# Kernel tuning notes

Hardware: AMD Instinct MI355X
Metric: run time of the kernel (lower is better)

Reference implementation:

```python
import jax, jax.numpy as jnp
import numpy as np

K = 8               # top-k frequencies
PRED_LEN = 96       # prediction_length
LOW_FREQ = 1        # low_frequency cutoff (drops DC)


def setup_inputs() -> dict:
    key = jax.random.key(0)
    x = jax.random.normal(key, (32, 2048, 64), dtype=jnp.float32)
    return {"x": x}


def reference(x):
    b, t, d = x.shape
    x_freq = jnp.fft.rfft(x, axis=1)                 # (b, t//2+1, d) complex
    freqs = jnp.fft.rfftfreq(t).astype(x.dtype)
    if t % 2 == 0:
        x_freq = x_freq[:, LOW_FREQ:-1]              # drop DC and Nyquist
        f = freqs[LOW_FREQ:-1]
    else:
        x_freq = x_freq[:, LOW_FREQ:]
        f = freqs[LOW_FREQ:]

    # top-k over frequency dim (axis=1), independently per (b, d)
    mag = jnp.abs(x_freq)                            # (b, F, d)
    _, idx = jax.lax.top_k(jnp.moveaxis(mag, 1, 2), K)  # (b, d, K), sorted desc
    idx = jnp.moveaxis(idx, 1, 2)                    # (b, K, d)
    x_k = jnp.take_along_axis(x_freq, idx, axis=1)   # (b, K, d) complex
    f_k = f[idx]                                     # (b, K, d)

    # extrapolate: add conjugate (negative) frequencies, then cos-sum
    x2 = jnp.concatenate([x_k, jnp.conj(x_k)], axis=1)  # (b, 2K, d)
    f2 = jnp.concatenate([f_k, -f_k], axis=1)           # (b, 2K, d)
    t_val = jnp.arange(t + PRED_LEN, dtype=x.dtype)     # (T,)
    amp = jnp.abs(x2) / t                               # (b, 2K, d)
    phase = jnp.angle(x2)                               # (b, 2K, d)
    # (b, 2K, T, d) broadcast intermediate, reduced over freq axis
    x_time = amp[:, :, None, :] * jnp.cos(
        2.0 * np.float32(np.pi) * f2[:, :, None, :] * t_val[None, None, :, None]
        + phase[:, :, None, :]
    )
    return x_time.sum(axis=1)                        # (b, t+PRED_LEN, d)
```

## Files before the change

### kernel.cpp

```cpp
#include <hip/hip_runtime.h>
#include <math.h>

#define BB 32
#define TT 2048
#define DD 64
#define PRED 96
#define TP (TT + PRED)
#define KTOP 8
#define NCAND 16
#define NSIG (BB * DD)
#define MARGIN 8e-4f
#define PI_D 3.14159265358979323846

__device__ __forceinline__ int physIdx(int idx) { return idx ^ ((idx >> 5) & 31); }

__device__ __forceinline__ int posOf(int k) {
    return ((k & 7) << 8) | (((k >> 3) & 7) << 5) | (((k >> 6) & 7) << 2) | (k >> 9);
}

__device__ __forceinline__ float2 cadd(float2 a, float2 b) { return make_float2(a.x + b.x, a.y + b.y); }
__device__ __forceinline__ float2 csub(float2 a, float2 b) { return make_float2(a.x - b.x, a.y - b.y); }
__device__ __forceinline__ float2 cmulni(float2 a) { return make_float2(a.y, -a.x); }
__device__ __forceinline__ float2 cmulpi(float2 a) { return make_float2(-a.y, a.x); }
__device__ __forceinline__ float2 cw8(float2 a) {
    const float s = 0.70710678118654752f;
    return make_float2(s * (a.x + a.y), s * (a.y - a.x));
}
__device__ __forceinline__ float2 cw83(float2 a) {
    const float s = 0.70710678118654752f;
    return make_float2(s * (a.y - a.x), -s * (a.x + a.y));
}
__device__ __forceinline__ float2 ctw(float2 a, int m) {
    const float rev = (float)m * (1.0f / 2048.0f);
    const float c = __builtin_amdgcn_cosf(rev);
    const float s = __builtin_amdgcn_sinf(rev);
    return make_float2(a.x * c + a.y * s, a.y * c - a.x * s);
}

__device__ __forceinline__ void radix8(float2* r) {
    float2 E0, E1, E2, E3, O0, O1, O2, O3;
    {
        float2 s0 = cadd(r[0], r[4]), s1 = csub(r[0], r[4]);
        float2 s2 = cadd(r[2], r[6]), s3 = csub(r[2], r[6]);
        E0 = cadd(s0, s2); E2 = csub(s0, s2);
        E1 = cadd(s1, cmulni(s3)); E3 = cadd(s1, cmulpi(s3));
    }
    {
        float2 s0 = cadd(r[1], r[5]), s1 = csub(r[1], r[5]);
        float2 s2 = cadd(r[3], r[7]), s3 = csub(r[3], r[7]);
        O0 = cadd(s0, s2); O2 = csub(s0, s2);
        O1 = cadd(s1, cmulni(s3)); O3 = cadd(s1, cmulpi(s3));
    }
    const float2 w1 = cw8(O1), w2 = cmulni(O2), w3 = cw83(O3);
    r[0] = cadd(E0, O0); r[4] = csub(E0, O0);
    r[1] = cadd(E1, w1); r[5] = csub(E1, w1);
    r[2] = cadd(E2, w2); r[6] = csub(E2, w2);
    r[3] = cadd(E3, w3); r[7] = csub(E3, w3);
}

__global__ __launch_bounds__(256) void fft_topk_kernel(const float* __restrict__ x,
                                                       int* __restrict__ idxw,
                                                       float* __restrict__ rew,
                                                       float* __restrict__ imw) {
    __shared__ float2 Z[TT];
    __shared__ int    candS[2][NCAND];
    __shared__ int    flagS[2];
    __shared__ double resR[2][NCAND], resI[2][NCAND], resM[2][NCAND];
    __shared__ double2 wA[32];
    __shared__ double2 wB[64];

    const int i    = blockIdx.x;
    const int xcd  = i & 7;
    const int slot = i >> 3;
    const int b    = xcd * 4 + (slot >> 5);
    const int dp   = slot & 31;
    const int t    = threadIdx.x;

    const float2* xv = (const float2*)x;
    const size_t base = (size_t)b * TT * (DD / 2) + dp;
    float2 r[8];
    #pragma unroll
    for (int q = 0; q < 8; ++q) r[q] = xv[base + (size_t)(t + 256 * q) * (DD / 2)];

    radix8(r);
    #pragma unroll
    for (int p = 1; p < 8; ++p) r[p] = ctw(r[p], (p * t) & (TT - 1));
    #pragma unroll
    for (int p = 0; p < 8; ++p) Z[physIdx(t + (p << 8))] = r[p];
    __syncthreads();

    const int S2 = (t >> 5) << 8, j2 = t & 31;
    #pragma unroll
    for (int p = 0; p < 8; ++p) r[p] = Z[physIdx(S2 + j2 + (p << 5))];
    radix8(r);
    #pragma unroll
    for (int p = 1; p < 8; ++p) r[p] = ctw(r[p], (8 * p * j2) & (TT - 1));
    #pragma unroll
    for (int p = 0; p < 8; ++p) Z[physIdx(S2 + j2 + (p << 5))] = r[p];
    __syncthreads();

    const int S3 = (t >> 2) << 5, j3 = t & 3;
    #pragma unroll
    for (int p = 0; p < 8; ++p) r[p] = Z[physIdx(S3 + j3 + (p << 2))];
    radix8(r);
    #pragma unroll
    for (int p = 1; p < 8; ++p) r[p] = ctw(r[p], (64 * p * j3) & (TT - 1));
    #pragma unroll
    for (int p = 0; p < 8; ++p) Z[physIdx(S3 + j3 + (p << 2))] = r[p];
    __syncthreads();

    #pragma unroll
    for (int g = 0; g < 2; ++g) {
        const int b4 = 8 * t + 4 * g;
        const float2 a = Z[physIdx(b4)],     bb = Z[physIdx(b4 + 1)];
        const float2 c = Z[physIdx(b4 + 2)], dd = Z[physIdx(b4 + 3)];
        const float2 s0 = cadd(a, c), s1 = csub(a, c);
        const float2 s2 = cadd(bb, dd), s3 = csub(bb, dd);
        Z[physIdx(b4)]     = cadd(s0, s2);
        Z[physIdx(b4 + 1)] = cadd(s1, cmulni(s3));
        Z[physIdx(b4 + 2)] = csub(s0, s2);
        Z[physIdx(b4 + 3)] = cadd(s1, cmulpi(s3));
    }
    __syncthreads();

    const int wv = t >> 6, lane = t & 63;
    if (wv < 2) {
        const int sig = wv;
        unsigned A[16];
        #pragma unroll
        for (int m = 0; m < 16; ++m) {
            const int k = lane + (m << 6);
            unsigned key = 0u;
            if (k != 0) {
                const float2 z = Z[physIdx(posOf(k))];
                const float2 y = Z[physIdx(posOf(TT - k))];
                float cr, ci;
                if (sig == 0) { cr = 0.5f * (z.x + y.x); ci = 0.5f * (z.y - y.y); }
                else          { cr = 0.5f * (z.y + y.y); ci = 0.5f * (y.x - z.x); }
                const float mg = cr * cr + ci * ci;
                key = (__float_as_uint(mg) & 0xFFFFF800u) | (unsigned)(2047 - k);
            }
            A[m] = key;
        }

        #pragma unroll
        for (int sz = 2; sz <= 16; sz <<= 1) {
            #pragma unroll
            for (int d = sz >> 1; d > 0; d >>= 1) {
                #pragma unroll
                for (int i2 = 0; i2 < 16; ++i2) {
                    const int j2i = i2 ^ d;
                    if (j2i > i2) {
                        const bool desc = ((i2 & sz) == 0);
                        const unsigned a = A[i2], b2 = A[j2i];
                        const unsigned mx = a > b2 ? a : b2;
                        const unsigned mn = a > b2 ? b2 : a;
                        A[i2]  = desc ? mx : mn;
                        A[j2i] = desc ? mn : mx;
                    }
                }
            }
        }

        #pragma unroll
        for (int off = 1; off < 64; off <<= 1) {
            unsigned Bv[16];
            #pragma unroll
            for (int i2 = 0; i2 < 16; ++i2)
                Bv[i2] = (unsigned)__shfl_xor((int)A[i2], off, 64);
            #pragma unroll
            for (int i2 = 0; i2 < 16; ++i2) {
                const unsigned o = Bv[15 - i2];
                A[i2] = A[i2] > o ? A[i2] : o;
            }
            #pragma unroll
            for (int d = 8; d > 0; d >>= 1) {
                #pragma unroll
                for (int i2 = 0; i2 < 16; ++i2) {
                    if ((i2 & d) == 0) {
                        const int j2i = i2 + d;
                        const unsigned a = A[i2], b2 = A[j2i];
                        A[i2]  = a > b2 ? a : b2;
                        A[j2i] = a > b2 ? b2 : a;
                    }
                }
            }
        }

        const float mf8 = __uint_as_float(A[7] & 0xFFFFF800u);
        const float mf9 = __uint_as_float(A[8] & 0xFFFFF800u);
        const int flg = (mf8 - mf9 <= MARGIN * mf8) ? 1 : 0;
        if (lane == 0) flagS[sig] = flg;

        unsigned myk = 0u;
        #pragma unroll
        for (int i2 = 0; i2 < 16; ++i2) myk = (lane == i2) ? A[i2] : myk;
        const int kwin = 2047 - (int)(myk & 0x7FFu);

        if (lane < NCAND) candS[sig][lane] = kwin;
        if (!flg && lane < KTOP) {
            const float2 z = Z[physIdx(posOf(kwin))];
            const float2 y = Z[physIdx(posOf(TT - kwin))];
            float cr, ci;
            if (sig == 0) { cr = 0.5f * (z.x + y.x); ci = 0.5f * (z.y - y.y); }
            else          { cr = 0.5f * (z.y + y.y); ci = 0.5f * (y.x - z.x); }
            const int s_sig = b * DD + 2 * dp + sig;
            idxw[s_sig * KTOP + lane] = kwin;
            rew[s_sig * KTOP + lane]  = cr * (2.0f / (float)TT);
            imw[s_sig * KTOP + lane]  = ci * (2.0f / (float)TT);
        }
    }
    __syncthreads();

    if (flagS[0] | flagS[1]) {
        #pragma unroll
        for (int q = 0; q < 8; ++q)
            Z[t + 256 * q] = xv[base + (size_t)(t + 256 * q) * (DD / 2)];
        if (t < 32) {
            const double th = -PI_D * (double)t / 16.0;
            wA[t] = make_double2(cos(th), sin(th));
        } else if (t < 96) {
            const int j = t - 32;
            const double th = -2.0 * PI_D * (double)j / (double)TT;
            wB[j] = make_double2(cos(th), sin(th));
        }
        __syncthreads();

        for (int sig = 0; sig < 2; ++sig) {
            if (!flagS[sig]) continue;
            for (int rr = wv; rr < NCAND; rr += 4) {
                const int k = candS[sig][rr];
                double ar = 0.0, ai = 0.0;
                for (int m = 0; m < TT / 64; ++m) {
                    const int n   = lane + 64 * m;
                    const int ix  = (k * n) & (TT - 1);
                    const double2 a  = wA[ix >> 6];
                    const double2 bw = wB[ix & 63];
                    const double wr = a.x * bw.x - a.y * bw.y;
                    const double wi = a.x * bw.y + a.y * bw.x;
                    const double xn = (sig == 0) ? (double)Z[n].x : (double)Z[n].y;
                    ar = fma(xn, wr, ar);
                    ai = fma(xn, wi, ai);
                }
                #pragma unroll
                for (int off = 32; off; off >>= 1) {
                    ar += __shfl_xor(ar, off, 64);
                    ai += __shfl_xor(ai, off, 64);
                }
                if (lane == 0) {
                    resR[sig][rr] = ar; resI[sig][rr] = ai;
                    resM[sig][rr] = ar * ar + ai * ai;
                }
            }
        }
        __syncthreads();

        if (t < 2 * NCAND) {
            const int sig = t / NCAND, rr = t % NCAND;
            if (flagS[sig]) {
                const double m = resM[sig][rr];
                const int    k = candS[sig][rr];
                int rank = 0;
                for (int r2 = 0; r2 < NCAND; ++r2) {
                    const double m2 = resM[sig][r2];
                    const int    k2 = candS[sig][r2];
                    if (m2 > m || (m2 == m && k2 < k)) ++rank;
                }
                if (rank < KTOP) {
                    const int s_sig = b * DD + 2 * dp + sig;
                    idxw[s_sig * KTOP + rank] = k;
                    rew[s_sig * KTOP + rank]  = (float)(resR[sig][rr] * (2.0 / (double)TT));
                    imw[s_sig * KTOP + rank]  = (float)(resI[sig][rr] * (2.0 / (double)TT));
                }
            }
        }
    }
}

__global__ __launch_bounds__(256) void synth_kernel(const int* __restrict__ idxw,
                                                    const float* __restrict__ rew,
                                                    const float* __restrict__ imw,
                                                    float* __restrict__ out) {
    const int NT   = (TP + 127) / 128;
    const int b    = blockIdx.x / NT;
    const int tile = blockIdx.x % NT;
    const int tid  = threadIdx.x;
    const int d    = tid & 63;
    const int tq   = tid >> 6;
    const int s    = b * DD + d;

    int   kk[KTOP];
    float rr[KTOP], ii[KTOP];
    int   jj[KTOP];
    #pragma unroll
    for (int p = 0; p < KTOP; ++p) {
        kk[p] = idxw[s * KTOP + p];
        rr[p] = rew[s * KTOP + p];
        ii[p] = imw[s * KTOP + p];
    }
    const int t0 = tile * 128 + tq * 32;
    #pragma unroll
    for (int p = 0; p < KTOP; ++p) jj[p] = (kk[p] * t0) & (TT - 1);

    const float invT = 1.0f / (float)TT;
    for (int i = 0; i < 32; ++i) {
        const int t = t0 + i;
        if (t < TP) {
            float acc = 0.0f;
            #pragma unroll
            for (int p = 0; p < KTOP; ++p) {
                const float rev = (float)jj[p] * invT;
                const float c  = __builtin_amdgcn_cosf(rev);
                const float sn = __builtin_amdgcn_sinf(rev);
                acc += rr[p] * c - ii[p] * sn;
            }
            out[((size_t)b * TP + t) * DD + d] = acc;
        }
        #pragma unroll
        for (int p = 0; p < KTOP; ++p) jj[p] = (jj[p] + kk[p]) & (TT - 1);
    }
}

extern "C" void kernel_launch(void* const* d_in, const int* in_sizes, int n_in,
                              void* d_out, int out_size, void* d_ws, size_t ws_size,
                              hipStream_t stream) {
    const float* x = (const float*)d_in[0];
    float* out = (float*)d_out;

    char* p = (char*)d_ws;
    int*   idxw = (int*)p;     p += (size_t)NSIG * KTOP * sizeof(int);
    float* rew  = (float*)p;   p += (size_t)NSIG * KTOP * sizeof(float);
    float* imw  = (float*)p;

    fft_topk_kernel<<<NSIG / 2, 256, 0, stream>>>(x, idxw, rew, imw);

    const int NT = (TP + 127) / 128;
    synth_kernel<<<BB * NT, 256, 0, stream>>>(idxw, rew, imw, out);
}
```

Before: 113.0 us.

## Compute each signal-pair FFT within one wavefront using registers and shuffles

```diff
diff --git a/kernel.cpp b/kernel.cpp
--- a/kernel.cpp
+++ b/kernel.cpp
@@ -7,29 +7,24 @@
 #define PRED 96
 #define TP (TT + PRED)
 #define KTOP 8
-#define NCAND 16
 #define NSIG (BB * DD)
 #define MARGIN 8e-4f
 #define PI_D 3.14159265358979323846
 
-__device__ __forceinline__ int physIdx(int idx) { return idx ^ ((idx >> 5) & 31); }
-
-__device__ __forceinline__ int posOf(int k) {
-    return ((k & 7) << 8) | (((k >> 3) & 7) << 5) | (((k >> 6) & 7) << 2) | (k >> 9);
-}
-
-__device__ __forceinline__ float2 cadd(float2 a, float2 b) { return make_float2(a.x + b.x, a.y + b.y); }
-__device__ __forceinline__ float2 csub(float2 a, float2 b) { return make_float2(a.x - b.x, a.y - b.y); }
-__device__ __forceinline__ float2 cmulni(float2 a) { return make_float2(a.y, -a.x); }
-__device__ __forceinline__ float2 cmulpi(float2 a) { return make_float2(-a.y, a.x); }
-__device__ __forceinline__ float2 cw8(float2 a) {
-    const float s = 0.70710678118654752f;
-    return make_float2(s * (a.x + a.y), s * (a.y - a.x));
-}
-__device__ __forceinline__ float2 cw83(float2 a) {
-    const float s = 0.70710678118654752f;
-    return make_float2(s * (a.y - a.x), -s * (a.x + a.y));
-}
+__device__ __forceinline__ int br6(int l) { return (int)(__brev((unsigned)l) >> 26); }
+static constexpr int BR5[32] = {0,16,8,24,4,20,12,28,2,18,10,26,6,22,14,30,
+                                1,17,9,25,5,21,13,29,3,19,11,27,7,23,15,31};
+static constexpr float C32T[16] = {
+    1.0f, 0.98078528040323044913f, 0.92387953251128675613f, 0.83146961230254523708f,
+    0.70710678118654752440f, 0.55557023301960222474f, 0.38268343236508977173f, 0.19509032201612826785f,
+    0.0f, -0.19509032201612826785f, -0.38268343236508977173f, -0.55557023301960222474f,
+    -0.70710678118654752440f, -0.83146961230254523708f, -0.92387953251128675613f, -0.98078528040323044913f};
+static constexpr float S32T[16] = {
+    0.0f, 0.19509032201612826785f, 0.38268343236508977173f, 0.55557023301960222474f,
+    0.70710678118654752440f, 0.83146961230254523708f, 0.92387953251128675613f, 0.98078528040323044913f,
+    1.0f, 0.98078528040323044913f, 0.92387953251128675613f, 0.83146961230254523708f,
+    0.70710678118654752440f, 0.55557023301960222474f, 0.38268343236508977173f, 0.19509032201612826785f};
+
 __device__ __forceinline__ float2 ctw(float2 a, int m) {
     const float rev = (float)m * (1.0f / 2048.0f);
     const float c = __builtin_amdgcn_cosf(rev);
@@ -37,110 +32,123 @@
     return make_float2(a.x * c + a.y * s, a.y * c - a.x * s);
 }
 
-__device__ __forceinline__ void radix8(float2* r) {
-    float2 E0, E1, E2, E3, O0, O1, O2, O3;
-    {
-        float2 s0 = cadd(r[0], r[4]), s1 = csub(r[0], r[4]);
-        float2 s2 = cadd(r[2], r[6]), s3 = csub(r[2], r[6]);
-        E0 = cadd(s0, s2); E2 = csub(s0, s2);
-        E1 = cadd(s1, cmulni(s3)); E3 = cadd(s1, cmulpi(s3));
-    }
-    {
-        float2 s0 = cadd(r[1], r[5]), s1 = csub(r[1], r[5]);
-        float2 s2 = cadd(r[3], r[7]), s3 = csub(r[3], r[7]);
-        O0 = cadd(s0, s2); O2 = csub(s0, s2);
-        O1 = cadd(s1, cmulni(s3)); O3 = cadd(s1, cmulpi(s3));
-    }
-    const float2 w1 = cw8(O1), w2 = cmulni(O2), w3 = cw83(O3);
-    r[0] = cadd(E0, O0); r[4] = csub(E0, O0);
-    r[1] = cadd(E1, w1); r[5] = csub(E1, w1);
-    r[2] = cadd(E2, w2); r[6] = csub(E2, w2);
-    r[3] = cadd(E3, w3); r[7] = csub(E3, w3);
-}
-
 __global__ __launch_bounds__(256) void fft_topk_kernel(const float* __restrict__ x,
                                                        int* __restrict__ idxw,
                                                        float* __restrict__ rew,
                                                        float* __restrict__ imw) {
-    __shared__ float2 Z[TT];
-    __shared__ int    candS[2][NCAND];
-    __shared__ int    flagS[2];
-    __shared__ double resR[2][NCAND], resI[2][NCAND], resM[2][NCAND];
-    __shared__ double2 wA[32];
-    __shared__ double2 wB[64];
-
-    const int i    = blockIdx.x;
-    const int xcd  = i & 7;
-    const int slot = i >> 3;
-    const int b    = xcd * 4 + (slot >> 5);
-    const int dp   = slot & 31;
+    __shared__ float SRe[4][2112];
+    __shared__ float SIm[4][2112];
+
     const int t    = threadIdx.x;
+    const int wv   = t >> 6, lane = t & 63;
+    const int bid  = blockIdx.x;
+    const int xcd  = bid & 7;
+    const int idx  = bid >> 3;
+    const int b    = xcd * 4 + (idx >> 3);
+    const int dp   = (idx & 7) * 4 + wv;
 
     const float2* xv = (const float2*)x;
-    const size_t base = (size_t)b * TT * (DD / 2) + dp;
-    float2 r[8];
-    #pragma unroll
-    for (int q = 0; q < 8; ++q) r[q] = xv[base + (size_t)(t + 256 * q) * (DD / 2)];
-
-    radix8(r);
-    #pragma unroll
-    for (int p = 1; p < 8; ++p) r[p] = ctw(r[p], (p * t) & (TT - 1));
-    #pragma unroll
-    for (int p = 0; p < 8; ++p) Z[physIdx(t + (p << 8))] = r[p];
+    const size_t xbase = (size_t)b * TT * (DD / 2) + dp;
+
+    float2 v[32];
+    #pragma unroll
+    for (int i = 0; i < 32; ++i)
+        v[i] = xv[xbase + (size_t)(64 * BR5[i] + lane) * (DD / 2)];
+
+    #pragma unroll
+    for (int s = 1; s <= 5; ++s) {
+        const int m = 1 << s, half = m >> 1, stepw = 32 >> s;
+        #pragma unroll
+        for (int g = 0; g < 32; g += m) {
+            #pragma unroll
+            for (int j = 0; j < half; ++j) {
+                const float c = C32T[j * stepw], sn = S32T[j * stepw];
+                const int i0 = g + j, i1 = i0 + half;
+                const float tr = c * v[i1].x + sn * v[i1].y;
+                const float ti = c * v[i1].y - sn * v[i1].x;
+                v[i1] = make_float2(v[i0].x - tr, v[i0].y - ti);
+                v[i0] = make_float2(v[i0].x + tr, v[i0].y + ti);
+            }
+        }
+    }
+
+    #pragma unroll
+    for (int q = 1; q < 32; ++q) v[q] = ctw(v[q], (lane * q) & (TT - 1));
+
+    {
+        const int rl = br6(lane);
+        #pragma unroll
+        for (int q = 0; q < 32; ++q) {
+            v[q].x = __shfl(v[q].x, rl, 64);
+            v[q].y = __shfl(v[q].y, rl, 64);
+        }
+    }
+    #pragma unroll
+    for (int s = 1; s <= 6; ++s) {
+        const int half = 1 << (s - 1);
+        const float rev = (float)(lane & (half - 1)) / (float)(1 << s);
+        const float wc  = __builtin_amdgcn_cosf(rev);
+        const float wsn = __builtin_amdgcn_sinf(rev);
+        const bool  hi  = (lane & half) != 0;
+        #pragma unroll
+        for (int q = 0; q < 32; ++q) {
+            float2 pv;
+            pv.x = __shfl_xor(v[q].x, half, 64);
+            pv.y = __shfl_xor(v[q].y, half, 64);
+            const float2 bsv = hi ? v[q] : pv;
+            const float2 asv = hi ? pv : v[q];
+            const float tr = wc * bsv.x + wsn * bsv.y;
+            const float ti = wc * bsv.y - wsn * bsv.x;
+            v[q] = hi ? make_float2(asv.x - tr, asv.y - ti)
+                      : make_float2(asv.x + tr, asv.y + ti);
+        }
+    }
+
+    #pragma unroll
+    for (int q = 0; q < 32; ++q) {
+        const int k = 32 * lane + q;
+        const int a = k + (k >> 5);
+        SRe[wv][a] = v[q].x;
+        SIm[wv][a] = v[q].y;
+    }
     __syncthreads();
 
-    const int S2 = (t >> 5) << 8, j2 = t & 31;
-    #pragma unroll
-    for (int p = 0; p < 8; ++p) r[p] = Z[physIdx(S2 + j2 + (p << 5))];
-    radix8(r);
-    #pragma unroll
-    for (int p = 1; p < 8; ++p) r[p] = ctw(r[p], (8 * p * j2) & (TT - 1));
-    #pragma unroll
-    for (int p = 0; p < 8; ++p) Z[physIdx(S2 + j2 + (p << 5))] = r[p];
-    __syncthreads();
-
-    const int S3 = (t >> 2) << 5, j3 = t & 3;
-    #pragma unroll
-    for (int p = 0; p < 8; ++p) r[p] = Z[physIdx(S3 + j3 + (p << 2))];
-    radix8(r);
-    #pragma unroll
-    for (int p = 1; p < 8; ++p) r[p] = ctw(r[p], (64 * p * j3) & (TT - 1));
-    #pragma unroll
-    for (int p = 0; p < 8; ++p) Z[physIdx(S3 + j3 + (p << 2))] = r[p];
-    __syncthreads();
-
-    #pragma unroll
-    for (int g = 0; g < 2; ++g) {
-        const int b4 = 8 * t + 4 * g;
-        const float2 a = Z[physIdx(b4)],     bb = Z[physIdx(b4 + 1)];
-        const float2 c = Z[physIdx(b4 + 2)], dd = Z[physIdx(b4 + 3)];
-        const float2 s0 = cadd(a, c), s1 = csub(a, c);
-        const float2 s2 = cadd(bb, dd), s3 = csub(bb, dd);
-        Z[physIdx(b4)]     = cadd(s0, s2);
-        Z[physIdx(b4 + 1)] = cadd(s1, cmulni(s3));
-        Z[physIdx(b4 + 2)] = csub(s0, s2);
-        Z[physIdx(b4 + 3)] = cadd(s1, cmulpi(s3));
-    }
-    __syncthreads();
-
-    const int wv = t >> 6, lane = t & 63;
-    if (wv < 2) {
-        const int sig = wv;
+    const int s_base = b * DD + 2 * dp;
+
+    int   flgv[2]  = {0, 0};
+    int   kwinv[2] = {0, 0};
+    unsigned bandmaskv[2] = {0, 0};
+
+    #pragma unroll
+    for (int sig = 0; sig < 2; ++sig) {
+        unsigned key[32];
+        if (lane < 32) {
+            #pragma unroll
+            for (int q = 0; q < 32; ++q) {
+                const int k = 32 * lane + q;
+                unsigned kk = 0u;
+                if (k != 0) {
+                    const int pk = TT - k, a2 = pk + (pk >> 5);
+                    const float yr = SRe[wv][a2], yi = SIm[wv][a2];
+                    const float zr = v[q].x, zi = v[q].y;
+                    float cr, ci;
+                    if (sig == 0) { cr = 0.5f * (zr + yr); ci = 0.5f * (zi - yi); }
+                    else          { cr = 0.5f * (zi + yi); ci = 0.5f * (yr - zr); }
+                    const float mg = cr * cr + ci * ci;
+                    kk = (__float_as_uint(mg) & 0xFFFFF800u) | (unsigned)(2047 - k);
+                }
+                key[q] = kk;
+            }
+        } else {
+            #pragma unroll
+            for (int q = 0; q < 32; ++q) key[q] = 0u;
+        }
+
         unsigned A[16];
         #pragma unroll
-        for (int m = 0; m < 16; ++m) {
-            const int k = lane + (m << 6);
-            unsigned key = 0u;
-            if (k != 0) {
-                const float2 z = Z[physIdx(posOf(k))];
-                const float2 y = Z[physIdx(posOf(TT - k))];
-                float cr, ci;
-                if (sig == 0) { cr = 0.5f * (z.x + y.x); ci = 0.5f * (z.y - y.y); }
-                else          { cr = 0.5f * (z.y + y.y); ci = 0.5f * (y.x - z.x); }
-                const float mg = cr * cr + ci * ci;
-                key = (__float_as_uint(mg) & 0xFFFFF800u) | (unsigned)(2047 - k);
-            }
-            A[m] = key;
+        for (int j = 0; j < 16; ++j) {
+            const unsigned u = (unsigned)__shfl((int)key[j + 16], lane & 31, 64);
+            A[j] = (lane < 32) ? key[j] : u;
         }
 
         #pragma unroll
@@ -153,15 +161,12 @@
                     if (j2i > i2) {
                         const bool desc = ((i2 & sz) == 0);
                         const unsigned a = A[i2], b2 = A[j2i];
-                        const unsigned mx = a > b2 ? a : b2;
-                        const unsigned mn = a > b2 ? b2 : a;
-                        A[i2]  = desc ? mx : mn;
-                        A[j2i] = desc ? mn : mx;
+                        const unsigned mx = a > b2 ? a : b2, mn = a > b2 ? b2 : a;
+                        A[i2] = desc ? mx : mn;  A[j2i] = desc ? mn : mx;
                     }
                 }
             }
         }
-
         #pragma unroll
         for (int off = 1; off < 64; off <<= 1) {
             unsigned Bv[16];
@@ -180,97 +185,109 @@
                     if ((i2 & d) == 0) {
                         const int j2i = i2 + d;
                         const unsigned a = A[i2], b2 = A[j2i];
-                        A[i2]  = a > b2 ? a : b2;
-                        A[j2i] = a > b2 ? b2 : a;
+                        A[i2] = a > b2 ? a : b2;  A[j2i] = a > b2 ? b2 : a;
                     }
                 }
             }
         }
 
-        const float mf8 = __uint_as_float(A[7] & 0xFFFFF800u);
-        const float mf9 = __uint_as_float(A[8] & 0xFFFFF800u);
-        const int flg = (mf8 - mf9 <= MARGIN * mf8) ? 1 : 0;
-        if (lane == 0) flagS[sig] = flg;
+        const float m8f = __uint_as_float(A[7] & 0xFFFFF800u);
+        unsigned bandmask = 0u;
+        #pragma unroll
+        for (int r = 0; r < 16; ++r) {
+            const float mr = __uint_as_float(A[r] & 0xFFFFF800u);
+            if (fabsf(mr - m8f) <= MARGIN * m8f) bandmask |= (1u << r);
+        }
+        const int flg = (bandmask != (1u << 7));
+        flgv[sig] = flg; bandmaskv[sig] = bandmask;
 
         unsigned myk = 0u;
         #pragma unroll
         for (int i2 = 0; i2 < 16; ++i2) myk = (lane == i2) ? A[i2] : myk;
         const int kwin = 2047 - (int)(myk & 0x7FFu);
-
-        if (lane < NCAND) candS[sig][lane] = kwin;
+        kwinv[sig] = kwin;
+
         if (!flg && lane < KTOP) {
-            const float2 z = Z[physIdx(posOf(kwin))];
-            const float2 y = Z[physIdx(posOf(TT - kwin))];
+            const int k = kwin, a1 = k + (k >> 5), pk = TT - k, a2 = pk + (pk >> 5);
+            const float zr = SRe[wv][a1], zi = SIm[wv][a1];
+            const float yr = SRe[wv][a2], yi = SIm[wv][a2];
             float cr, ci;
-            if (sig == 0) { cr = 0.5f * (z.x + y.x); ci = 0.5f * (z.y - y.y); }
-            else          { cr = 0.5f * (z.y + y.y); ci = 0.5f * (y.x - z.x); }
-            const int s_sig = b * DD + 2 * dp + sig;
-            idxw[s_sig * KTOP + lane] = kwin;
+            if (sig == 0) { cr = 0.5f * (zr + yr); ci = 0.5f * (zi - yi); }
+            else          { cr = 0.5f * (zi + yi); ci = 0.5f * (yr - zr); }
+            const int s_sig = s_base + sig;
+            idxw[s_sig * KTOP + lane] = k;
             rew[s_sig * KTOP + lane]  = cr * (2.0f / (float)TT);
             imw[s_sig * KTOP + lane]  = ci * (2.0f / (float)TT);
         }
     }
-    __syncthreads();
-
-    if (flagS[0] | flagS[1]) {
-        #pragma unroll
-        for (int q = 0; q < 8; ++q)
-            Z[t + 256 * q] = xv[base + (size_t)(t + 256 * q) * (DD / 2)];
-        if (t < 32) {
-            const double th = -PI_D * (double)t / 16.0;
-            wA[t] = make_double2(cos(th), sin(th));
-        } else if (t < 96) {
-            const int j = t - 32;
-            const double th = -2.0 * PI_D * (double)j / (double)TT;
-            wB[j] = make_double2(cos(th), sin(th));
-        }
-        __syncthreads();
+
+    if (flgv[0] | flgv[1]) {
+        float2 sv[32];
+        #pragma unroll
+        for (int m = 0; m < 32; ++m)
+            sv[m] = xv[xbase + (size_t)(lane + 64 * m) * (DD / 2)];
+        const double thA = -2.0 * PI_D * (double)lane / 64.0;
+        const double thB = -2.0 * PI_D * (double)lane / (double)TT;
+        const double wac = cos(thA), was = sin(thA);
+        const double wbc = cos(thB), wbs = sin(thB);
 
         for (int sig = 0; sig < 2; ++sig) {
-            if (!flagS[sig]) continue;
-            for (int rr = wv; rr < NCAND; rr += 4) {
-                const int k = candS[sig][rr];
+            if (!flgv[sig]) continue;
+            const unsigned bandmask = bandmaskv[sig];
+            const int lo = (int)__builtin_ctz(bandmask);
+            double myM = 0.0, myR = 0.0, myI = 0.0;
+            for (int r = 0; r < 16; ++r) {
+                if (!((bandmask >> r) & 1u)) continue;
+                const int kr = __shfl(kwinv[sig], r, 64);
                 double ar = 0.0, ai = 0.0;
-                for (int m = 0; m < TT / 64; ++m) {
-                    const int n   = lane + 64 * m;
-                    const int ix  = (k * n) & (TT - 1);
-                    const double2 a  = wA[ix >> 6];
-                    const double2 bw = wB[ix & 63];
-                    const double wr = a.x * bw.x - a.y * bw.y;
-                    const double wi = a.x * bw.y + a.y * bw.x;
-                    const double xn = (sig == 0) ? (double)Z[n].x : (double)Z[n].y;
-                    ar = fma(xn, wr, ar);
-                    ai = fma(xn, wi, ai);
+                for (int m = 0; m < 32; ++m) {
+                    const int n  = lane + 64 * m;
+                    const int mm = (n * kr) & (TT - 1);
+                    const double qc = __shfl(wac, mm >> 5, 64);
+                    const double qs = __shfl(was, mm >> 5, 64);
+                    const double rc = __shfl(wbc, mm & 31, 64);
+                    const double rs = __shfl(wbs, mm & 31, 64);
+                    const double wr = qc * rc - qs * rs;
+                    const double wi = qc * rs + qs * rc;
+                    const double xs = (sig == 0) ? (double)sv[m].x : (double)sv[m].y;
+                    ar = fma(xs, wr, ar);
+                    ai = fma(xs, wi, ai);
                 }
                 #pragma unroll
                 for (int off = 32; off; off >>= 1) {
                     ar += __shfl_xor(ar, off, 64);
                     ai += __shfl_xor(ai, off, 64);
                 }
-                if (lane == 0) {
-                    resR[sig][rr] = ar; resI[sig][rr] = ai;
-                    resM[sig][rr] = ar * ar + ai * ai;
-                }
-            }
-        }
-        __syncthreads();
-
-        if (t < 2 * NCAND) {
-            const int sig = t / NCAND, rr = t % NCAND;
-            if (flagS[sig]) {
-                const double m = resM[sig][rr];
-                const int    k = candS[sig][rr];
-                int rank = 0;
-                for (int r2 = 0; r2 < NCAND; ++r2) {
-                    const double m2 = resM[sig][r2];
-                    const int    k2 = candS[sig][r2];
-                    if (m2 > m || (m2 == m && k2 < k)) ++rank;
-                }
-                if (rank < KTOP) {
-                    const int s_sig = b * DD + 2 * dp + sig;
-                    idxw[s_sig * KTOP + rank] = k;
-                    rew[s_sig * KTOP + rank]  = (float)(resR[sig][rr] * (2.0 / (double)TT));
-                    imw[s_sig * KTOP + rank]  = (float)(resI[sig][rr] * (2.0 / (double)TT));
+                if (lane == r) { myM = ar * ar + ai * ai; myR = ar; myI = ai; }
+            }
+            int rank = lane;
+            if (lane < 16 && ((bandmask >> lane) & 1u)) {
+                int rb = 0;
+                for (int r2 = 0; r2 < 16; ++r2) {
+                    if (!((bandmask >> r2) & 1u)) continue;
+                    const double om = __shfl(myM, r2, 64);
+                    const int    ok = __shfl(kwinv[sig], r2, 64);
+                    if (r2 != lane &&
+                        (om > myM || (om == myM && ok < kwinv[sig]))) ++rb;
+                }
+                rank = lo + rb;
+            }
+            if (lane < 16 && rank < KTOP) {
+                const int s_sig = s_base + sig;
+                const int k = kwinv[sig];
+                idxw[s_sig * KTOP + rank] = k;
+                if ((bandmask >> lane) & 1u) {
+                    rew[s_sig * KTOP + rank] = (float)(myR * (2.0 / (double)TT));
+                    imw[s_sig * KTOP + rank] = (float)(myI * (2.0 / (double)TT));
+                } else {
+                    const int a1 = k + (k >> 5), pk = TT - k, a2 = pk + (pk >> 5);
+                    const float zr = SRe[wv][a1], zi = SIm[wv][a1];
+                    const float yr = SRe[wv][a2], yi = SIm[wv][a2];
+                    float cr, ci;
+                    if (sig == 0) { cr = 0.5f * (zr + yr); ci = 0.5f * (zi - yi); }
+                    else          { cr = 0.5f * (zi + yi); ci = 0.5f * (yr - zr); }
+                    rew[s_sig * KTOP + rank] = cr * (2.0f / (float)TT);
+                    imw[s_sig * KTOP + rank] = ci * (2.0f / (float)TT);
                 }
             }
         }
@@ -332,7 +349,7 @@
     float* rew  = (float*)p;   p += (size_t)NSIG * KTOP * sizeof(float);
     float* imw  = (float*)p;
 
-    fft_topk_kernel<<<NSIG / 2, 256, 0, stream>>>(x, idxw, rew, imw);
+    fft_topk_kernel<<<NSIG / 8, 256, 0, stream>>>(x, idxw, rew, imw);
 
     const int NT = (TP + 127) / 128;
     synth_kernel<<<BB * NT, 256, 0, stream>>>(idxw, rew, imw, out);
```

Measured after the change: 121.6 us. 1.08x slower.
